# Kernel tuning notes

Hardware: AMD Instinct MI355X
Metric: run time of the kernel (lower is better)

The kernel has to match this reference:

```python
import jax, jax.numpy as jnp
import numpy as np

B, N, C = 4, 4096, 96  # batch, HW patches, channels


def setup_inputs() -> dict:
    key = jax.random.key(0)
    k1, k2, k3 = jax.random.split(key, 3)
    x = jax.random.normal(k1, (B, N + 1, C), dtype=jnp.float32)
    edge = jax.random.normal(k2, (B, N, N), dtype=jnp.float32)
    # theta: Linear(C, 1, bias=False), kaiming_normal init
    theta_w = jax.random.normal(k3, (1, C), dtype=jnp.float32) * np.float32(np.sqrt(2.0 / C))
    return {"x": x, "edge": edge, "theta_w": theta_w,
            "reduction_ratio": 4, "pooling_patch_size": 4}


def reference(x, edge, theta_w, reduction_ratio, pooling_patch_size):
    ps = int(pooling_patch_size)
    tk = ps // int(reduction_ratio)  # top_k per patch
    b, n1, c = x.shape
    nodes = x[:, 1:]                                  # (B, N, C)
    s_edge = jax.nn.sigmoid(edge)                     # (B, N, N)
    s_nodes = jax.nn.sigmoid(nodes)                   # (B, N, C)
    edge_dot_node = jnp.einsum('bnm,bmc->bnc', s_edge, s_nodes)  # (B, N, C)
    scores = jnp.einsum('bnc,oc->bno', edge_dot_node, theta_w)[..., 0]  # (B, N)
    num_patches = n1 // ps                            # matches torch loop count
    scores_p = scores[:, :num_patches * ps].reshape(b, num_patches, ps)
    vals, idx = jax.lax.top_k(scores_p, tk)           # (B, P, tk), idx relative in [0, ps)
    vals = vals.reshape(b, num_patches * tk)          # (B, P*tk) mask values
    idx = idx.reshape(b, num_patches * tk)            # (B, P*tk) relative indices (faithful to source)
    gathered = jnp.take_along_axis(nodes, idx[..., None], axis=1)  # (B, P*tk, C)
    pooled = vals[..., None] * gathered + gathered    # mask-multiply-add
    out = jnp.concatenate([x[:, :1], pooled], axis=1)  # (B, 1+P*tk, C)
    return out
```

## Files before the change

### kernel.cpp

```cpp
#include <hip/hip_runtime.h>
#include <hip/hip_bf16.h>

#define BB 4
#define NN 4096
#define CC 96
#define N1 4097
#define OUTROWS 1025
#define THREADS 512
#define ROWS_PER_BLK 64
#define PATCHES_PER_BLK 16
#define BLKS_PER_B 64
#define NBLK (BB * BLKS_PER_B)

__device__ __forceinline__ float fast_sigmoid(float v) {
    return __builtin_amdgcn_rcpf(1.0f + __expf(-v));
}

__global__ __launch_bounds__(THREADS) void fused_pool_kernel(
    const float* __restrict__ x, const float* __restrict__ edge,
    const float* __restrict__ theta, float* __restrict__ out)
{
    __shared__ float t_lds[NN];
    __shared__ float partial[8][4];
    __shared__ float s_lds[ROWS_PER_BLK];

    const int tid     = threadIdx.x;
    const int b       = blockIdx.x >> 6;
    const int blkInB  = blockIdx.x & 63;
    const int rowbase = blkInB * ROWS_PER_BLK;

    const float* xb = x + (size_t)b * N1 * CC;

    if (blkInB == 0 && tid < CC)
        out[(size_t)b * OUTROWS * CC + tid] = xb[tid];

    for (int k = 0; k < NN / THREADS; ++k) {
        int m = k * THREADS + tid;
        const float* xr = xb + (size_t)(m + 1) * CC;
        float acc = 0.0f;
        #pragma unroll
        for (int c4 = 0; c4 < CC / 4; ++c4) {
            float4 xv = *reinterpret_cast<const float4*>(xr + c4 * 4);
            float4 tw = *reinterpret_cast<const float4*>(theta + c4 * 4);
            acc += fast_sigmoid(xv.x) * tw.x;
            acc += fast_sigmoid(xv.y) * tw.y;
            acc += fast_sigmoid(xv.z) * tw.z;
            acc += fast_sigmoid(xv.w) * tw.w;
        }
        t_lds[m] = acc;
    }
    __syncthreads();

    const int grp      = tid >> 8;
    const int gtid     = tid & 255;
    const int gwave    = gtid >> 6;
    const int glane    = gtid & 63;
    const int growbase = rowbase + grp * 32;
    const float* eb = edge + ((size_t)b * NN + growbase) * NN;

    for (int q = 0; q < 8; ++q) {
        float a0 = 0.f, a1 = 0.f, a2 = 0.f, a3 = 0.f;
        const float* e0 = eb + (size_t)(q * 4 + 0) * NN;
        const float* e1 = eb + (size_t)(q * 4 + 1) * NN;
        const float* e2 = eb + (size_t)(q * 4 + 2) * NN;
        const float* e3 = eb + (size_t)(q * 4 + 3) * NN;
        #pragma unroll
        for (int it = 0; it < 4; ++it) {
            int idx = it * 1024 + gtid * 4;
            float4 tv = *reinterpret_cast<const float4*>(&t_lds[idx]);
            float4 v0 = *reinterpret_cast<const float4*>(e0 + idx);
            float4 v1 = *reinterpret_cast<const float4*>(e1 + idx);
            float4 v2 = *reinterpret_cast<const float4*>(e2 + idx);
            float4 v3 = *reinterpret_cast<const float4*>(e3 + idx);
            a0 += tv.x * fast_sigmoid(v0.x); a0 += tv.y * fast_sigmoid(v0.y);
            a0 += tv.z * fast_sigmoid(v0.z); a0 += tv.w * fast_sigmoid(v0.w);
            a1 += tv.x * fast_sigmoid(v1.x); a1 += tv.y * fast_sigmoid(v1.y);
            a1 += tv.z * fast_sigmoid(v1.z); a1 += tv.w * fast_sigmoid(v1.w);
            a2 += tv.x * fast_sigmoid(v2.x); a2 += tv.y * fast_sigmoid(v2.y);
            a2 += tv.z * fast_sigmoid(v2.z); a2 += tv.w * fast_sigmoid(v2.w);
            a3 += tv.x * fast_sigmoid(v3.x); a3 += tv.y * fast_sigmoid(v3.y);
            a3 += tv.z * fast_sigmoid(v3.z); a3 += tv.w * fast_sigmoid(v3.w);
        }
        #pragma unroll
        for (int off = 32; off > 0; off >>= 1) {
            a0 += __shfl_down(a0, off, 64);
            a1 += __shfl_down(a1, off, 64);
            a2 += __shfl_down(a2, off, 64);
            a3 += __shfl_down(a3, off, 64);
        }
        if (glane == 0) {
            int w = grp * 4 + gwave;
            partial[w][0] = a0; partial[w][1] = a1;
            partial[w][2] = a2; partial[w][3] = a3;
        }
        __syncthreads();
        if (gtid < 4) {
            int r = gtid;
            int w0 = grp * 4;
            s_lds[grp * 32 + q * 4 + r] =
                partial[w0 + 0][r] + partial[w0 + 1][r] +
                partial[w0 + 2][r] + partial[w0 + 3][r];
        }
        __syncthreads();
    }

    const int wave = tid >> 6;
    const int lane = tid & 63;
    for (int pp = wave; pp < PATCHES_PER_BLK; pp += 8) {
        float s0 = s_lds[pp * 4 + 0], s1 = s_lds[pp * 4 + 1];
        float s2 = s_lds[pp * 4 + 2], s3 = s_lds[pp * 4 + 3];
        float best = s0; int bi = 0;
        if (s1 > best) { best = s1; bi = 1; }
        if (s2 > best) { best = s2; bi = 2; }
        if (s3 > best) { best = s3; bi = 3; }
        const float* g = xb + (size_t)(bi + 1) * CC;
        float scale = best + 1.0f;
        float* orow = out + ((size_t)b * OUTROWS + 1 +
                             blkInB * PATCHES_PER_BLK + pp) * CC;
        orow[lane] = scale * g[lane];
        if (lane < CC - 64) orow[lane + 64] = scale * g[lane + 64];
    }
}

extern "C" void kernel_launch(void* const* d_in, const int* in_sizes, int n_in,
                              void* d_out, int out_size, void* d_ws, size_t ws_size,
                              hipStream_t stream) {
    const float* x     = (const float*)d_in[0];
    const float* edge  = (const float*)d_in[1];
    const float* theta = (const float*)d_in[2];
    float* out = (float*)d_out;

    fused_pool_kernel<<<NBLK, THREADS, 0, stream>>>(x, edge, theta, out);
}
```

Measured before the change: 405.8 us.

## Assign one edge row per wave and drop cross-wave LDS reductions

Doubles the block size to 1024 threads and makes each of 16 waves reduce whole edge rows alone, using only intra-wave shuffles. This removes the per-row-group partial array and the two __syncthreads per iteration, leaving a single barrier before the top-k and gather stage. Each wave now handles exactly one patch in that final stage. With more threads per block, the t precompute loop runs fewer iterations per thread, but register pressure under the larger launch bound may limit occupancy.

Result: slower. 454.0 us (+11.9%).

```diff
diff --git a/kernel.cpp b/kernel.cpp
--- a/kernel.cpp
+++ b/kernel.cpp
@@ -6,11 +6,10 @@
 #define CC 96
 #define N1 4097
 #define OUTROWS 1025
-#define THREADS 512
+#define THREADS 1024
 #define ROWS_PER_BLK 64
 #define PATCHES_PER_BLK 16
-#define BLKS_PER_B 64
-#define NBLK (BB * BLKS_PER_B)
+#define NBLK 256
 
 __device__ __forceinline__ float fast_sigmoid(float v) {
     return __builtin_amdgcn_rcpf(1.0f + __expf(-v));
@@ -21,7 +20,6 @@
     const float* __restrict__ theta, float* __restrict__ out)
 {
     __shared__ float t_lds[NN];
-    __shared__ float partial[8][4];
     __shared__ float s_lds[ROWS_PER_BLK];
 
     const int tid     = threadIdx.x;
@@ -34,6 +32,7 @@
     if (blkInB == 0 && tid < CC)
         out[(size_t)b * OUTROWS * CC + tid] = xb[tid];
 
+    #pragma unroll
     for (int k = 0; k < NN / THREADS; ++k) {
         int m = k * THREADS + tid;
         const float* xr = xb + (size_t)(m + 1) * CC;
@@ -51,35 +50,33 @@
     }
     __syncthreads();
 
-    const int grp      = tid >> 8;
-    const int gtid     = tid & 255;
-    const int gwave    = gtid >> 6;
-    const int glane    = gtid & 63;
-    const int growbase = rowbase + grp * 32;
-    const float* eb = edge + ((size_t)b * NN + growbase) * NN;
+    const int wave = tid >> 6;
+    const int lane = tid & 63;
+    const float* eb = edge + ((size_t)b * NN + rowbase) * NN;
 
-    for (int q = 0; q < 8; ++q) {
+    for (int q = 0; q < 4; ++q) {
+        const int r = wave * 4 + q;
+        const float* er = eb + (size_t)r * NN;
         float a0 = 0.f, a1 = 0.f, a2 = 0.f, a3 = 0.f;
-        const float* e0 = eb + (size_t)(q * 4 + 0) * NN;
-        const float* e1 = eb + (size_t)(q * 4 + 1) * NN;
-        const float* e2 = eb + (size_t)(q * 4 + 2) * NN;
-        const float* e3 = eb + (size_t)(q * 4 + 3) * NN;
         #pragma unroll
         for (int it = 0; it < 4; ++it) {
-            int idx = it * 1024 + gtid * 4;
-            float4 tv = *reinterpret_cast<const float4*>(&t_lds[idx]);
-            float4 v0 = *reinterpret_cast<const float4*>(e0 + idx);
-            float4 v1 = *reinterpret_cast<const float4*>(e1 + idx);
-            float4 v2 = *reinterpret_cast<const float4*>(e2 + idx);
-            float4 v3 = *reinterpret_cast<const float4*>(e3 + idx);
-            a0 += tv.x * fast_sigmoid(v0.x); a0 += tv.y * fast_sigmoid(v0.y);
-            a0 += tv.z * fast_sigmoid(v0.z); a0 += tv.w * fast_sigmoid(v0.w);
-            a1 += tv.x * fast_sigmoid(v1.x); a1 += tv.y * fast_sigmoid(v1.y);
-            a1 += tv.z * fast_sigmoid(v1.z); a1 += tv.w * fast_sigmoid(v1.w);
-            a2 += tv.x * fast_sigmoid(v2.x); a2 += tv.y * fast_sigmoid(v2.y);
-            a2 += tv.z * fast_sigmoid(v2.z); a2 += tv.w * fast_sigmoid(v2.w);
-            a3 += tv.x * fast_sigmoid(v3.x); a3 += tv.y * fast_sigmoid(v3.y);
-            a3 += tv.z * fast_sigmoid(v3.z); a3 += tv.w * fast_sigmoid(v3.w);
+            const int base = it * 1024 + lane * 4;
+            float4 e0 = *reinterpret_cast<const float4*>(er + base);
+            float4 e1 = *reinterpret_cast<const float4*>(er + base + 256);
+            float4 e2 = *reinterpret_cast<const float4*>(er + base + 512);
+            float4 e3 = *reinterpret_cast<const float4*>(er + base + 768);
+            float4 t0 = *reinterpret_cast<const float4*>(&t_lds[base]);
+            float4 t1 = *reinterpret_cast<const float4*>(&t_lds[base + 256]);
+            float4 t2 = *reinterpret_cast<const float4*>(&t_lds[base + 512]);
+            float4 t3 = *reinterpret_cast<const float4*>(&t_lds[base + 768]);
+            a0 += t0.x * fast_sigmoid(e0.x); a0 += t0.y * fast_sigmoid(e0.y);
+            a0 += t0.z * fast_sigmoid(e0.z); a0 += t0.w * fast_sigmoid(e0.w);
+            a1 += t1.x * fast_sigmoid(e1.x); a1 += t1.y * fast_sigmoid(e1.y);
+            a1 += t1.z * fast_sigmoid(e1.z); a1 += t1.w * fast_sigmoid(e1.w);
+            a2 += t2.x * fast_sigmoid(e2.x); a2 += t2.y * fast_sigmoid(e2.y);
+            a2 += t2.z * fast_sigmoid(e2.z); a2 += t2.w * fast_sigmoid(e2.w);
+            a3 += t3.x * fast_sigmoid(e3.x); a3 += t3.y * fast_sigmoid(e3.y);
+            a3 += t3.z * fast_sigmoid(e3.z); a3 += t3.w * fast_sigmoid(e3.w);
         }
         #pragma unroll
         for (int off = 32; off > 0; off >>= 1) {
@@ -88,25 +85,12 @@
             a2 += __shfl_down(a2, off, 64);
             a3 += __shfl_down(a3, off, 64);
         }
-        if (glane == 0) {
-            int w = grp * 4 + gwave;
-            partial[w][0] = a0; partial[w][1] = a1;
-            partial[w][2] = a2; partial[w][3] = a3;
-        }
-        __syncthreads();
-        if (gtid < 4) {
-            int r = gtid;
-            int w0 = grp * 4;
-            s_lds[grp * 32 + q * 4 + r] =
-                partial[w0 + 0][r] + partial[w0 + 1][r] +
-                partial[w0 + 2][r] + partial[w0 + 3][r];
-        }
-        __syncthreads();
+        if (lane == 0) s_lds[r] = ((a0 + a1) + a2) + a3;
     }
+    __syncthreads();
 
-    const int wave = tid >> 6;
-    const int lane = tid & 63;
-    for (int pp = wave; pp < PATCHES_PER_BLK; pp += 8) {
+    {
+        const int pp = wave;
         float s0 = s_lds[pp * 4 + 0], s1 = s_lds[pp * 4 + 1];
         float s2 = s_lds[pp * 4 + 2], s3 = s_lds[pp * 4 + 3];
         float best = s0; int bi = 0;
```
